# Performance work log

Hardware: AMD Instinct MI355X
Metric: run time of the kernel (lower is better)

The kernel has to match this reference:

```python
import jax, jax.numpy as jnp
import numpy as np

B, S, H, NH = 4, 2048, 1024, 16
D = H // NH  # head dim = 64


def setup_inputs() -> dict:
    key = jax.random.key(0)
    ks = jax.random.split(key, 4)
    scale = 1.0 / np.sqrt(H)
    return {
        "hidden_states": jax.random.normal(ks[0], (B, S, H), dtype=jnp.float32),
        "attention_mask": jnp.zeros((B, 1, 1, S), dtype=jnp.float32),
        "Wq": jax.random.normal(ks[1], (H, H), dtype=jnp.float32) * scale,
        "bq": jnp.zeros((H,), dtype=jnp.float32),
        "Wk": jax.random.normal(ks[2], (H, H), dtype=jnp.float32) * scale,
        "bk": jnp.zeros((H,), dtype=jnp.float32),
        "Wv": jax.random.normal(ks[3], (H, H), dtype=jnp.float32) * scale,
        "bv": jnp.zeros((H,), dtype=jnp.float32),
    }


def _split_heads(x):
    # [B, S, H] -> [B, NH, S, D]
    return x.reshape(B, S, NH, D).transpose(0, 2, 1, 3)


def reference(hidden_states, attention_mask, Wq, bq, Wk, bk, Wv, bv):
    # NOTE: faithful to source quirk: key/value projections are applied to the
    # query projection output (mixed_query_layer), not to keyvalue_states.
    mixed_q = hidden_states @ Wq.T + bq            # [B, S, H]
    q = _split_heads(mixed_q)                       # [B, NH, S, D]
    k = _split_heads(mixed_q @ Wk.T + bk)           # [B, NH, S, D]
    v = _split_heads(mixed_q @ Wv.T + bv)           # [B, NH, S, D]

    scores = jnp.einsum("bhqd,bhkd->bhqk", q, k) / jnp.sqrt(jnp.float32(D))
    scores = scores + attention_mask                # additive mask [B,1,1,S]
    probs = jax.nn.softmax(scores, axis=-1)         # dropout = identity (eval)
    ctx = jnp.einsum("bhqk,bhkd->bhqd", probs, v)   # [B, NH, S, D]
    ctx = ctx.transpose(0, 2, 1, 3).reshape(B, S, H)
    return ctx
```

## Files before the change

### kernel.cpp

```cpp
#include <hip/hip_runtime.h>
#include <stdint.h>

typedef float  f32x4  __attribute__((ext_vector_type(4)));
typedef float  f32x16 __attribute__((ext_vector_type(16)));
typedef short  s16x8  __attribute__((ext_vector_type(8)));
typedef unsigned int u32x4 __attribute__((ext_vector_type(4)));
typedef unsigned short u16;
typedef u16    u16x4 __attribute__((ext_vector_type(4)));

#define SLEN 2048
#define HDIM 1024
#define NHEAD 16
#define DHEAD 64
#define BATCH 4
#define LOG2E 1.44269504088896340736f
#define SC2   0.18033688011111772f
#define ISC2  5.5451774444795623f

__device__ __forceinline__ u16 f2bf(float f) {
  uint32_t u = __builtin_bit_cast(uint32_t, f);
  u += 0x7FFFu + ((u >> 16) & 1u);
  return (u16)(u >> 16);
}

__device__ __forceinline__ uint32_t cvtpk2(float a, float b) {
  uint32_t r;
  asm("v_cvt_pk_bf16_f32 %0, %1, %2" : "=v"(r) : "v"(a), "v"(b));
  return r;
}

__device__ __forceinline__ void gld_lds16(const void* g, void* l) {
  __builtin_amdgcn_global_load_lds(
      (const __attribute__((address_space(1))) unsigned int*)g,
      (__attribute__((address_space(3))) unsigned int*)l, 16, 0, 0);
}

__global__ __launch_bounds__(256) void prep_all(
    const float4* __restrict__ hs, const float4* __restrict__ W0,
    const float4* __restrict__ W1, const float4* __restrict__ W2,
    const float* __restrict__ mask, const float* __restrict__ bq,
    u16* __restrict__ HSb, u16* __restrict__ O0, u16* __restrict__ O1,
    u16* __restrict__ O2, float* __restrict__ m2, float* __restrict__ bqs,
    float* __restrict__ flagp) {
  const int bid = blockIdx.x, tid = threadIdx.x;
  if (bid < 8192) {
    int i = bid * 256 + tid;
    float4 v = hs[i];
    u16x4 o;
    o.x = f2bf(v.x); o.y = f2bf(v.y); o.z = f2bf(v.z); o.w = f2bf(v.w);
    *(u16x4*)(HSb + (size_t)i * 4) = o;
  } else if (bid < 11264) {
    int zz = (bid - 8192) >> 10;
    int i = ((bid - 8192) & 1023) * 256 + tid;
    const float4* in = zz == 0 ? W0 : (zz == 1 ? W1 : W2);
    u16* out = zz == 0 ? O0 : (zz == 1 ? O1 : O2);
    const float sc = zz == 0 ? SC2 : ISC2;
    float4 v = in[i];
    u16x4 o;
    o.x = f2bf(v.x * sc); o.y = f2bf(v.y * sc);
    o.z = f2bf(v.z * sc); o.w = f2bf(v.w * sc);
    *(u16x4*)(out + (size_t)i * 4) = o;
  } else if (bid < 11296) {
    int i = (bid - 11264) * 256 + tid;
    m2[i] = mask[i] * LOG2E;
  } else if (bid < 11297) {
#pragma unroll
    for (int k = 0; k < 4; ++k) bqs[tid + k * 256] = bq[tid + k * 256] * SC2;
  } else {
    float a = 0.f;
#pragma unroll
    for (int k = 0; k < 32; ++k) a += __builtin_fabsf(mask[tid + k * 256]);
    int nz = __any(a != 0.f) ? 1 : 0;
    if ((tid & 63) == 0) flagp[tid >> 6] = (float)nz;
  }
}

__device__ __forceinline__ void gemm_body(const u16* __restrict__ A,
                                          const u16* __restrict__ W,
                                          const float* __restrict__ bias,
                                          u16* __restrict__ C, int mode) {
  __shared__ u16 As[4][128 * 32];
  __shared__ u16 Bs[4][128 * 32];
  const int tid = threadIdx.x;
  const int lane = tid & 63;
  const int w = tid >> 6;
  const int wr = w >> 1, wc = w & 1;
  const int flat = blockIdx.x + blockIdx.y * 8;
  const int swz = (flat & 7) * 64 + (flat >> 3);
  const int brow = (swz >> 3) * 128;
  const int bcol = (swz & 7) * 128;
  const int l15 = lane & 15, l4 = lane >> 4;

  const int r0 = tid >> 2, c0 = tid & 3;
  const int sc0 = c0 ^ ((r0 >> 1) & 3);
  const int r1 = r0 + 64;
  const int sc1 = c0 ^ ((r1 >> 1) & 3);
  const u16* Abase = A + (size_t)brow * HDIM;
  const u16* Bbase = W + (size_t)bcol * HDIM;

  f32x4 acc[4][4];
#pragma unroll
  for (int m = 0; m < 4; ++m)
#pragma unroll
    for (int n = 0; n < 4; ++n) acc[m][n] = f32x4{0.f, 0.f, 0.f, 0.f};

  auto stage = [&](int s) {
    const int slot = s & 3;
    const int k0 = s * 32;
    gld_lds16(Abase + (size_t)r0 * HDIM + k0 + sc0 * 8, &As[slot][tid * 8]);
    gld_lds16(Abase + (size_t)r1 * HDIM + k0 + sc1 * 8,
              &As[slot][(tid + 256) * 8]);
    gld_lds16(Bbase + (size_t)r0 * HDIM + k0 + sc0 * 8, &Bs[slot][tid * 8]);
    gld_lds16(Bbase + (size_t)r1 * HDIM + k0 + sc1 * 8,
              &Bs[slot][(tid + 256) * 8]);
  };

  auto compute = [&](int s) {
    const int slot = s & 3;
    s16x8 af[4], bf[4];
#pragma unroll
    for (int m = 0; m < 4; ++m) {
      const int row = wr * 64 + m * 16 + l15;
      const int pc = l4 ^ ((row >> 1) & 3);
      af[m] = *(const s16x8*)&As[slot][row * 32 + pc * 8];
    }
#pragma unroll
    for (int n = 0; n < 4; ++n) {
      const int row = wc * 64 + n * 16 + l15;
      const int pc = l4 ^ ((row >> 1) & 3);
      bf[n] = *(const s16x8*)&Bs[slot][row * 32 + pc * 8];
    }
    if (s < 29) stage(s + 3);
#pragma unroll
    for (int m = 0; m < 4; ++m)
#pragma unroll
      for (int n = 0; n < 4; ++n)
        acc[m][n] = __builtin_amdgcn_mfma_f32_16x16x32_bf16(af[m], bf[n],
                                                            acc[m][n], 0, 0, 0);
  };

  stage(0); stage(1); stage(2);

#pragma unroll 1
  for (int s = 0; s < 30; ++s) {
    asm volatile("s_waitcnt vmcnt(8)" ::: "memory");
    asm volatile("s_barrier" ::: "memory");
    compute(s);
  }
  asm volatile("s_waitcnt vmcnt(4)" ::: "memory");
  asm volatile("s_barrier" ::: "memory");
  compute(30);
  asm volatile("s_waitcnt vmcnt(0)" ::: "memory");
  asm volatile("s_barrier" ::: "memory");
  compute(31);

#pragma unroll
  for (int n = 0; n < 4; ++n) {
    int col = bcol + wc * 64 + n * 16 + l15;
    float bv = bias[col];
#pragma unroll
    for (int m = 0; m < 4; ++m) {
      int row0 = brow + wr * 64 + m * 16 + l4 * 4;
      if (mode == 0) {
#pragma unroll
        for (int j = 0; j < 4; ++j)
          C[(size_t)(row0 + j) * HDIM + col] = f2bf(acc[m][n][j] + bv);
      } else {
        u16x4 o;
#pragma unroll
        for (int j = 0; j < 4; ++j) o[j] = f2bf(acc[m][n][j] + bv);
        *(u16x4*)(C + (size_t)(((row0 >> 11) << 10) + col) * SLEN +
                  (row0 & (SLEN - 1))) = o;
      }
    }
  }
}

__global__ __launch_bounds__(256) void gemm_bt(const u16* __restrict__ A,
                                               const u16* __restrict__ W,
                                               const float* __restrict__ bias,
                                               u16* __restrict__ C) {
  gemm_body(A, W, bias, C, 0);
}

__global__ __launch_bounds__(256) void gemm_kv(const u16* __restrict__ A,
                                               const u16* __restrict__ Wk,
                                               const float* __restrict__ bk,
                                               u16* __restrict__ K,
                                               const u16* __restrict__ Wv,
                                               const float* __restrict__ bv,
                                               u16* __restrict__ Vt) {
  if (blockIdx.z == 0) gemm_body(A, Wk, bk, K, 0);
  else                 gemm_body(A, Wv, bv, Vt, 1);
}

__global__ __launch_bounds__(512, 4) void attn_kernel(
    const u16* __restrict__ Qs, const u16* __restrict__ Kb,
    const u16* __restrict__ Vtg, const float* __restrict__ m2g,
    const float* __restrict__ flagp, float* __restrict__ out) {
  __shared__ u16 Ks[2][64 * 64];
  __shared__ u16 Vts[2][64 * 64];

  const int tid = threadIdx.x;
  const int lane = tid & 63;
  const int w = tid >> 6;
  const int bid = blockIdx.x;
  const int swz = (bid & 7) * 64 + (bid >> 3);
  const int qt = swz & 7;
  const int bh = swz >> 3;
  const int b = bh >> 4, h = bh & 15;
  const int l31 = lane & 31;
  const int h1 = lane >> 5;

  const float4 fl = *(const float4*)flagp;
  const bool mz = (fl.x == 0.f && fl.y == 0.f && fl.z == 0.f && fl.w == 0.f);

  const int q0 = qt * 256 + w * 32;
  s16x8 qf[4];
  {
    const u16* qp = Qs + (size_t)(b * SLEN + q0 + l31) * HDIM + h * DHEAD + h1 * 8;
#pragma unroll
    for (int dch = 0; dch < 4; ++dch) qf[dch] = *(const s16x8*)(qp + dch * 16);
  }

  const s16x8 onesf = {(short)0x3F80, (short)0x3F80, (short)0x3F80,
                       (short)0x3F80, (short)0x3F80, (short)0x3F80,
                       (short)0x3F80, (short)0x3F80};

  const float zf = fl.x * 0.0f;
  f32x16 zc;
#pragma unroll
  for (int i = 0; i < 16; ++i) zc[i] = zf;

  const int r0 = tid >> 3, c0 = tid & 7;
  const int cl0 = c0 ^ (r0 & 7);
  const u16* Kbase = Kb + (size_t)(b * SLEN) * HDIM + h * DHEAD;
  const u16* Vbase = Vtg + (size_t)bh * 64 * SLEN;
  const float* mbase = m2g + b * SLEN;
  const u16* KstA = Kbase + (size_t)r0 * HDIM + cl0 * 8;
  const u16* VstA = Vbase + (size_t)r0 * SLEN + cl0 * 8;

  f32x16 acc0{}, acc1{}, acc_s{};

  auto stage = [&](u16* Kd, u16* Vd, int kbn) {
    const size_t ko = (size_t)kbn * 64 * HDIM;
    const int vo = kbn * 64;
    gld_lds16(KstA + ko, Kd + tid * 8);
    gld_lds16(VstA + vo, Vd + tid * 8);
  };

  auto tile = [&](const u16* Kc, const u16* Vc, int kb) {
    uint32_t W[16];
#pragma unroll
    for (int kblk = 0; kblk < 2; ++kblk) {
      f32x16 cinit;
      if (mz) {
        cinit = zc;
      } else {
#pragma unroll
        for (int g = 0; g < 4; ++g) {
          float4 mk =
              *(const float4*)(mbase + kb * 64 + kblk * 32 + g * 8 + h1 * 4);
          cinit[4 * g + 0] = mk.x; cinit[4 * g + 1] = mk.y;
          cinit[4 * g + 2] = mk.z; cinit[4 * g + 3] = mk.w;
        }
      }
      const int row = kblk * 32 + l31;
      __builtin_amdgcn_s_setprio(1);
      f32x16 sT;
      {
        const int ch = h1 ^ (row & 7);
        s16x8 kf = *(const s16x8*)(Kc + row * 64 + ch * 8);
        sT = __builtin_amdgcn_mfma_f32_32x32x16_bf16(kf, qf[0], cinit, 0, 0, 0);
      }
#pragma unroll
      for (int dch = 1; dch < 4; ++dch) {
        const int ch = (dch * 2 + h1) ^ (row & 7);
        s16x8 kf = *(const s16x8*)(Kc + row * 64 + ch * 8);
        sT = __builtin_amdgcn_mfma_f32_32x32x16_bf16(kf, qf[dch], sT, 0, 0, 0);
      }
      __builtin_amdgcn_s_setprio(0);
#pragma unroll
      for (int g = 0; g < 4; ++g) {
        float p0 = __builtin_amdgcn_exp2f(sT[4 * g + 0]);
        float p1 = __builtin_amdgcn_exp2f(sT[4 * g + 1]);
        float p2 = __builtin_amdgcn_exp2f(sT[4 * g + 2]);
        float p3 = __builtin_amdgcn_exp2f(sT[4 * g + 3]);
        W[kblk * 8 + 2 * g]     = cvtpk2(p0, p1);
        W[kblk * 8 + 2 * g + 1] = cvtpk2(p2, p3);
      }
    }

#pragma unroll
    for (int c = 0; c < 4; ++c) {
#pragma unroll
      for (int e = 0; e < 2; ++e) {
        uint32_t a = W[4 * c + e], bb = W[4 * c + 2 + e];
        asm("v_permlane32_swap_b32 %0, %1" : "+v"(a), "+v"(bb));
        W[4 * c + e] = a;
        W[4 * c + 2 + e] = bb;
      }
    }

    __builtin_amdgcn_s_setprio(1);
#pragma unroll
    for (int c = 0; c < 4; ++c) {
      u32x4 t = {W[4 * c], W[4 * c + 1], W[4 * c + 2], W[4 * c + 3]};
      s16x8 af = __builtin_bit_cast(s16x8, t);
      const int ch = (c * 2 + h1) ^ (l31 & 7);
      s16x8 vf0 = *(const s16x8*)(Vc + l31 * 64 + ch * 8);
      s16x8 vf1 = *(const s16x8*)(Vc + (32 + l31) * 64 + ch * 8);
      acc0 = __builtin_amdgcn_mfma_f32_32x32x16_bf16(af, vf0, acc0, 0, 0, 0);
      acc1 = __builtin_amdgcn_mfma_f32_32x32x16_bf16(af, vf1, acc1, 0, 0, 0);
      acc_s = __builtin_amdgcn_mfma_f32_32x32x16_bf16(af, onesf, acc_s, 0, 0, 0);
    }
    __builtin_amdgcn_s_setprio(0);
  };

  stage(&Ks[0][0], &Vts[0][0], 0);
  __syncthreads();

#pragma unroll 1
  for (int t = 0; t < 15; ++t) {
    stage(&Ks[1][0], &Vts[1][0], 2 * t + 1);
    tile(&Ks[0][0], &Vts[0][0], 2 * t);
    __syncthreads();
    stage(&Ks[0][0], &Vts[0][0], 2 * t + 2);
    tile(&Ks[1][0], &Vts[1][0], 2 * t + 1);
    __syncthreads();
  }
  stage(&Ks[1][0], &Vts[1][0], 31);
  tile(&Ks[0][0], &Vts[0][0], 30);
  __syncthreads();
  tile(&Ks[1][0], &Vts[1][0], 31);

  const size_t obase = (size_t)(b * SLEN + q0);
#pragma unroll
  for (int r = 0; r < 16; ++r) {
    const int qr = (r & 3) + 8 * (r >> 2) + 4 * h1;
    const float si = 1.0f / acc_s[r];
    float* op = out + (obase + qr) * HDIM + h * DHEAD;
    op[l31]      = acc0[r] * si;
    op[32 + l31] = acc1[r] * si;
  }
}

extern "C" void kernel_launch(void* const* d_in, const int* in_sizes, int n_in,
                              void* d_out, int out_size, void* d_ws, size_t ws_size,
                              hipStream_t stream) {
  (void)in_sizes; (void)n_in; (void)out_size; (void)ws_size;
  const float* hs   = (const float*)d_in[0];
  const float* mask = (const float*)d_in[1];
  const float* Wq   = (const float*)d_in[2];
  const float* bq   = (const float*)d_in[3];
  const float* Wk   = (const float*)d_in[4];
  const float* bk   = (const float*)d_in[5];
  const float* Wv   = (const float*)d_in[6];
  const float* bv   = (const float*)d_in[7];
  float* out = (float*)d_out;

  char* ws = (char*)d_ws;
  const size_t MTOK = (size_t)BATCH * SLEN;
  const size_t MB = 1024 * 1024;
  u16* HSb = (u16*)ws;
  u16* Wqs = (u16*)(ws + 16 * MB);
  u16* Wks = (u16*)(ws + 18 * MB);
  u16* Wvs = (u16*)(ws + 20 * MB);
  u16* Qs  = (u16*)(ws + 22 * MB);
  u16* Kb  = (u16*)(ws + 38 * MB);
  u16* Vt  = (u16*)(ws + 54 * MB);
  float* m2  = (float*)(ws + 70 * MB);
  float* bqs = m2 + MTOK;
  float* flg = bqs + 1024;

  prep_all<<<11298, 256, 0, stream>>>((const float4*)hs, (const float4*)Wq,
                                      (const float4*)Wk, (const float4*)Wv,
                                      mask, bq, HSb, Wqs, Wks, Wvs, m2, bqs, flg);

  dim3 gg(HDIM / 128, MTOK / 128);
  gemm_bt<<<gg, 256, 0, stream>>>(HSb, Wqs, bqs, Qs);
  dim3 gkv(HDIM / 128, MTOK / 128, 2);
  gemm_kv<<<gkv, 256, 0, stream>>>(Qs, Wks, bk, Kb, Wvs, bv, Vt);

  attn_kernel<<<BATCH * NHEAD * (SLEN / 256), 512, 0, stream>>>(Qs, Kb, Vt, m2,
                                                                flg, out);
}
```

Measured before the change: 166.7 us.

## Triple-buffer K/V tiles with vmcnt waits and compute row sums via VALU

The attention kernel moves from a double-buffered LDS pipeline with __syncthreads to a three-stage ring. Each tile issues the prefetch two tiles ahead and waits with s_waitcnt vmcnt(2) plus a raw s_barrier, so global-to-LDS loads overlap more with compute. The softmax denominator, previously an extra MFMA against a ones vector, is now a per-lane VALU sum of the exp values, reduced across half-waves by shuffle. This frees MFMA issue slots and an accumulator, at the cost of 50% more LDS (which may reduce occupancy under the 512x4 launch bound) and relying on hand-written waitcnt for correctness.

```diff
diff --git a/kernel.cpp b/kernel.cpp
--- a/kernel.cpp
+++ b/kernel.cpp
@@ -198,8 +198,8 @@
     const u16* __restrict__ Qs, const u16* __restrict__ Kb,
     const u16* __restrict__ Vtg, const float* __restrict__ m2g,
     const float* __restrict__ flagp, float* __restrict__ out) {
-  __shared__ u16 Ks[2][64 * 64];
-  __shared__ u16 Vts[2][64 * 64];
+  __shared__ u16 Ks[3][64 * 64];
+  __shared__ u16 Vts[3][64 * 64];
 
   const int tid = threadIdx.x;
   const int lane = tid & 63;
@@ -223,14 +223,7 @@
     for (int dch = 0; dch < 4; ++dch) qf[dch] = *(const s16x8*)(qp + dch * 16);
   }
 
-  const s16x8 onesf = {(short)0x3F80, (short)0x3F80, (short)0x3F80,
-                       (short)0x3F80, (short)0x3F80, (short)0x3F80,
-                       (short)0x3F80, (short)0x3F80};
-
   const float zf = fl.x * 0.0f;
-  f32x16 zc;
-#pragma unroll
-  for (int i = 0; i < 16; ++i) zc[i] = zf;
 
   const int r0 = tid >> 3, c0 = tid & 7;
   const int cl0 = c0 ^ (r0 & 7);
@@ -240,22 +233,25 @@
   const u16* KstA = Kbase + (size_t)r0 * HDIM + cl0 * 8;
   const u16* VstA = Vbase + (size_t)r0 * SLEN + cl0 * 8;
 
-  f32x16 acc0{}, acc1{}, acc_s{};
+  f32x16 acc0{}, acc1{};
+  float s_sm = 0.f;
 
   auto stage = [&](u16* Kd, u16* Vd, int kbn) {
-    const size_t ko = (size_t)kbn * 64 * HDIM;
-    const int vo = kbn * 64;
-    gld_lds16(KstA + ko, Kd + tid * 8);
-    gld_lds16(VstA + vo, Vd + tid * 8);
+    gld_lds16(KstA + (size_t)kbn * 64 * HDIM, Kd + tid * 8);
+    gld_lds16(VstA + kbn * 64, Vd + tid * 8);
   };
 
-  auto tile = [&](const u16* Kc, const u16* Vc, int kb) {
+  auto tile = [&](const u16* Kc, const u16* Vc, int kb, u16* Kn, u16* Vn,
+                  bool doSt) {
+    if (doSt) stage(Kn, Vn, kb + 2);
     uint32_t W[16];
+    float ts = 0.f;
 #pragma unroll
     for (int kblk = 0; kblk < 2; ++kblk) {
       f32x16 cinit;
       if (mz) {
-        cinit = zc;
+#pragma unroll
+        for (int i = 0; i < 16; ++i) cinit[i] = zf;
       } else {
 #pragma unroll
         for (int g = 0; g < 4; ++g) {
@@ -266,19 +262,17 @@
         }
       }
       const int row = kblk * 32 + l31;
+      s16x8 kf[4];
+#pragma unroll
+      for (int dch = 0; dch < 4; ++dch) {
+        const int ch = (dch * 2 + h1) ^ (row & 7);
+        kf[dch] = *(const s16x8*)(Kc + row * 64 + ch * 8);
+      }
       __builtin_amdgcn_s_setprio(1);
-      f32x16 sT;
-      {
-        const int ch = h1 ^ (row & 7);
-        s16x8 kf = *(const s16x8*)(Kc + row * 64 + ch * 8);
-        sT = __builtin_amdgcn_mfma_f32_32x32x16_bf16(kf, qf[0], cinit, 0, 0, 0);
-      }
-#pragma unroll
-      for (int dch = 1; dch < 4; ++dch) {
-        const int ch = (dch * 2 + h1) ^ (row & 7);
-        s16x8 kf = *(const s16x8*)(Kc + row * 64 + ch * 8);
-        sT = __builtin_amdgcn_mfma_f32_32x32x16_bf16(kf, qf[dch], sT, 0, 0, 0);
-      }
+      f32x16 sT = __builtin_amdgcn_mfma_f32_32x32x16_bf16(kf[0], qf[0], cinit, 0, 0, 0);
+#pragma unroll
+      for (int dch = 1; dch < 4; ++dch)
+        sT = __builtin_amdgcn_mfma_f32_32x32x16_bf16(kf[dch], qf[dch], sT, 0, 0, 0);
       __builtin_amdgcn_s_setprio(0);
 #pragma unroll
       for (int g = 0; g < 4; ++g) {
@@ -286,10 +280,12 @@
         float p1 = __builtin_amdgcn_exp2f(sT[4 * g + 1]);
         float p2 = __builtin_amdgcn_exp2f(sT[4 * g + 2]);
         float p3 = __builtin_amdgcn_exp2f(sT[4 * g + 3]);
+        ts += (p0 + p1) + (p2 + p3);
         W[kblk * 8 + 2 * g]     = cvtpk2(p0, p1);
         W[kblk * 8 + 2 * g + 1] = cvtpk2(p2, p3);
       }
     }
+    s_sm += ts;
 
 #pragma unroll
     for (int c = 0; c < 4; ++c) {
@@ -312,33 +308,37 @@
       s16x8 vf1 = *(const s16x8*)(Vc + (32 + l31) * 64 + ch * 8);
       acc0 = __builtin_amdgcn_mfma_f32_32x32x16_bf16(af, vf0, acc0, 0, 0, 0);
       acc1 = __builtin_amdgcn_mfma_f32_32x32x16_bf16(af, vf1, acc1, 0, 0, 0);
-      acc_s = __builtin_amdgcn_mfma_f32_32x32x16_bf16(af, onesf, acc_s, 0, 0, 0);
     }
     __builtin_amdgcn_s_setprio(0);
   };
 
+#define WAIT2 do { asm volatile("s_waitcnt vmcnt(2)" ::: "memory"); \
+                   asm volatile("s_barrier" ::: "memory"); } while (0)
+#define WAIT0 do { asm volatile("s_waitcnt vmcnt(0)" ::: "memory"); \
+                   asm volatile("s_barrier" ::: "memory"); } while (0)
+
   stage(&Ks[0][0], &Vts[0][0], 0);
-  __syncthreads();
+  stage(&Ks[1][0], &Vts[1][0], 1);
 
 #pragma unroll 1
-  for (int t = 0; t < 15; ++t) {
-    stage(&Ks[1][0], &Vts[1][0], 2 * t + 1);
-    tile(&Ks[0][0], &Vts[0][0], 2 * t);
-    __syncthreads();
-    stage(&Ks[0][0], &Vts[0][0], 2 * t + 2);
-    tile(&Ks[1][0], &Vts[1][0], 2 * t + 1);
-    __syncthreads();
-  }
-  stage(&Ks[1][0], &Vts[1][0], 31);
-  tile(&Ks[0][0], &Vts[0][0], 30);
-  __syncthreads();
-  tile(&Ks[1][0], &Vts[1][0], 31);
-
+  for (int t = 0; t < 30; t += 3) {
+    WAIT2; tile(&Ks[0][0], &Vts[0][0], t,     &Ks[2][0], &Vts[2][0], true);
+    WAIT2; tile(&Ks[1][0], &Vts[1][0], t + 1, &Ks[0][0], &Vts[0][0], true);
+    WAIT2; tile(&Ks[2][0], &Vts[2][0], t + 2, &Ks[1][0], &Vts[1][0], true);
+  }
+  WAIT2; tile(&Ks[0][0], &Vts[0][0], 30, nullptr, nullptr, false);
+  WAIT0; tile(&Ks[1][0], &Vts[1][0], 31, nullptr, nullptr, false);
+
+#undef WAIT2
+#undef WAIT0
+
+  s_sm += __shfl_xor(s_sm, 32);
+  const float sinv = 1.0f / s_sm;
   const size_t obase = (size_t)(b * SLEN + q0);
 #pragma unroll
   for (int r = 0; r < 16; ++r) {
     const int qr = (r & 3) + 8 * (r >> 2) + 4 * h1;
-    const float si = 1.0f / acc_s[r];
+    const float si = __shfl(sinv, qr);
     float* op = out + (obase + qr) * HDIM + h * DHEAD;
     op[l31]      = acc0[r] * si;
     op[32 + l31] = acc1[r] * si;
```

After: 261.0 us. +56.5%, slower.
